# Performance work log

Measured on AMD Instinct MI355X. Metric: run time of the kernel, lower is better.

Reference implementation:

```python
import jax, jax.numpy as jnp
import numpy as np

NUM_HEADS = 12
D_MODEL = 768
D_K = D_MODEL // NUM_HEADS


def setup_inputs() -> dict:
    key = jax.random.key(0)
    k0, k1, k2, k3, k4 = jax.random.split(key, 5)
    B, S = 4, 2048
    scale = 1.0 / np.sqrt(D_MODEL)
    return {
        "x": jax.random.normal(k0, (B, S, D_MODEL), dtype=jnp.float32),
        "wq": jax.random.normal(k1, (D_MODEL, D_MODEL), dtype=jnp.float32) * scale,
        "wk": jax.random.normal(k2, (D_MODEL, D_MODEL), dtype=jnp.float32) * scale,
        "wv": jax.random.normal(k3, (D_MODEL, D_MODEL), dtype=jnp.float32) * scale,
        "wo": jax.random.normal(k4, (D_MODEL, D_MODEL), dtype=jnp.float32) * scale,
    }


def reference(x, wq, wk, wv, wo):
    # x: [B, S, d_model]; weights are torch Linear weights [out, in], applied as x @ W^T
    B, S, _ = x.shape
    q = (x @ wq.T).reshape(B, S, NUM_HEADS, D_K).transpose(0, 2, 1, 3)  # [B,H,S,dk]
    k = (x @ wk.T).reshape(B, S, NUM_HEADS, D_K).transpose(0, 2, 1, 3)
    v = (x @ wv.T).reshape(B, S, NUM_HEADS, D_K).transpose(0, 2, 1, 3)
    # Note: original calls scaled_dot_product_attention(queries, keys, values),
    # whose body computes (first_arg @ second_arg^T) => standard Q K^T scores.
    scores = jnp.einsum("bhqd,bhkd->bhqk", q, k) / jnp.sqrt(jnp.float32(D_K))
    causal_mask = jnp.triu(jnp.ones((S, S), dtype=bool), k=1)  # True above diagonal
    scores = jnp.where(causal_mask, -jnp.inf, scores)
    probs = jax.nn.softmax(scores, axis=-1)  # stable max-subtracted softmax, as in source
    attn = jnp.einsum("bhqk,bhkd->bhqd", probs, v)  # [B,H,S,dk]
    attn = attn.transpose(0, 2, 1, 3).reshape(B, S, D_MODEL)
    return attn @ wo.T
```

## Files before the change

kernel.cpp:

```cpp
#include <hip/hip_runtime.h>
#include <stdint.h>

#define DMODEL 768
#define NHEADS 12
#define DK 64
#define BATCH 4
#define SEQ 2048
#define MTOK (BATCH*SEQ)

typedef float f32x4 __attribute__((ext_vector_type(4)));
typedef short bf16x8 __attribute__((ext_vector_type(8)));
typedef unsigned short u16;

__device__ __forceinline__ u16 f2bf(float f) {
  uint32_t u = __float_as_uint(f);
  u += 0x7FFFu + ((u >> 16) & 1u);
  return (u16)(u >> 16);
}

#define GLDS16(g, l) __builtin_amdgcn_global_load_lds( \
    (const __attribute__((address_space(1))) unsigned int*)(g), \
    (__attribute__((address_space(3))) unsigned int*)(l), 16, 0, 0)

__global__ void cvt_kernel(const float* __restrict__ src, u16* __restrict__ dst, int n4) {
  int i = blockIdx.x * blockDim.x + threadIdx.x;
  if (i >= n4) return;
  float4 v = reinterpret_cast<const float4*>(src)[i];
  ushort4 o;
  o.x = f2bf(v.x); o.y = f2bf(v.y); o.z = f2bf(v.z); o.w = f2bf(v.w);
  reinterpret_cast<ushort4*>(dst)[i] = o;
}

__global__ void cvt_w4(const float* __restrict__ w0, const float* __restrict__ w1,
                       const float* __restrict__ w2, const float* __restrict__ w3,
                       u16* __restrict__ dst, int n4) {
  int i = blockIdx.x * blockDim.x + threadIdx.x;
  if (i >= n4) return;
  const float* src = (blockIdx.y == 0) ? w0 : (blockIdx.y == 1) ? w1 : (blockIdx.y == 2) ? w2 : w3;
  float4 v = reinterpret_cast<const float4*>(src)[i];
  ushort4 o;
  o.x = f2bf(v.x); o.y = f2bf(v.y); o.z = f2bf(v.z); o.w = f2bf(v.w);
  reinterpret_cast<ushort4*>(dst + (size_t)blockIdx.y * DMODEL * DMODEL)[i] = o;
}

#define BM 128
#define BN 128
#define BK 32

__device__ __forceinline__ void gemm_loop(const u16* __restrict__ A, const u16* __restrict__ W,
                                          int bm, int bn, int t, u16* As, u16* Ws,
                                          f32x4 (&acc)[2][4]) {
  const int lane = t & 63;
  const int wave = t >> 6;
  const int r16 = lane & 15, g = lane >> 4;
  const int wr = (wave >> 1) * 32;
  const int wc = (wave & 1) * 64;
  const int crow = t >> 2;
  const int cchunk = (t & 3) ^ ((t >> 3) & 3);
  const size_t aoff = (size_t)(bm + crow) * DMODEL + cchunk * 8;
  const size_t woff = (size_t)(bn + crow) * DMODEL + cchunk * 8;

  GLDS16(A + aoff, As + t * 8);
  GLDS16(W + woff, Ws + t * 8);
  __syncthreads();

  const int NK = DMODEL / BK;
  for (int kt = 0; kt < NK; ++kt) {
    const int cur = kt & 1;
    if (kt + 1 < NK) {
      GLDS16(A + aoff + (size_t)(kt + 1) * BK, As + (cur ^ 1) * 4096 + t * 8);
      GLDS16(W + woff + (size_t)(kt + 1) * BK, Ws + (cur ^ 1) * 4096 + t * 8);
    }
    bf16x8 af[2], bfr[4];
#pragma unroll
    for (int m = 0; m < 2; ++m) {
      const int row = wr + m * 16 + r16;
      af[m] = *reinterpret_cast<const bf16x8*>(&As[cur * 4096 + row * 32 + ((g ^ ((row >> 1) & 3)) * 8)]);
    }
#pragma unroll
    for (int n = 0; n < 4; ++n) {
      const int row = wc + n * 16 + r16;
      bfr[n] = *reinterpret_cast<const bf16x8*>(&Ws[cur * 4096 + row * 32 + ((g ^ ((row >> 1) & 3)) * 8)]);
    }
#pragma unroll
    for (int m = 0; m < 2; ++m)
#pragma unroll
      for (int n = 0; n < 4; ++n)
        acc[m][n] = __builtin_amdgcn_mfma_f32_16x16x32_bf16(af[m], bfr[n], acc[m][n], 0, 0, 0);
    __syncthreads();
  }
}

__launch_bounds__(512)
__global__ void qkv_gemm(const u16* __restrict__ A, const u16* __restrict__ wAll,
                         u16* __restrict__ Qw, u16* __restrict__ Kw, u16* __restrict__ Vtw) {
  __shared__ __align__(16) u16 As[2 * BM * BK];
  __shared__ __align__(16) u16 Ws[2 * BN * BK];
  const int t = threadIdx.x;
  const int lane = t & 63, wave = t >> 6;
  const int r16 = lane & 15, g = lane >> 4;
  const int bm = blockIdx.x * BM, bn = blockIdx.y * BN;
  const int z = blockIdx.z;
  const u16* W = wAll + (size_t)z * DMODEL * DMODEL;
  const int wr = (wave >> 1) * 32, wc = (wave & 1) * 64;

  f32x4 acc[2][4] = {};
  gemm_loop(A, W, bm, bn, t, As, Ws, acc);

  if (z <= 1) {
    u16* Qo = (z == 0) ? Qw : Kw;
    const float scl = (z == 0) ? 0.125f : 1.0f;
#pragma unroll
    for (int m = 0; m < 2; ++m) {
      const int gi0 = bm + wr + m * 16 + g * 4;
#pragma unroll
      for (int n = 0; n < 4; ++n) {
        const int gj = bn + wc + n * 16 + r16;
        const int h = gj >> 6, dc = gj & 63;
#pragma unroll
        for (int r = 0; r < 4; ++r) {
          const int gi = gi0 + r;
          const int b_ = gi >> 11, s = gi & 2047;
          Qo[((size_t)((b_ * NHEADS + h) * SEQ + s) << 6) + dc] = f2bf(acc[m][n][r] * scl);
        }
      }
    }
  } else {
#pragma unroll
    for (int m = 0; m < 2; ++m) {
      const int gi0 = bm + wr + m * 16 + g * 4;
      const int b_ = gi0 >> 11, s0 = gi0 & 2047;
#pragma unroll
      for (int n = 0; n < 4; ++n) {
        const int gj = bn + wc + n * 16 + r16;
        const int h = gj >> 6, dc = gj & 63;
        ushort4 pk;
        pk.x = f2bf(acc[m][n][0]); pk.y = f2bf(acc[m][n][1]);
        pk.z = f2bf(acc[m][n][2]); pk.w = f2bf(acc[m][n][3]);
        *reinterpret_cast<ushort4*>(Vtw + ((size_t)((b_ * NHEADS + h) * DK + dc) * SEQ + s0)) = pk;
      }
    }
  }
}

__launch_bounds__(512)
__global__ void out_gemm(const u16* __restrict__ A, const u16* __restrict__ W,
                         float* __restrict__ C) {
  __shared__ __align__(16) u16 As[2 * BM * BK];
  __shared__ __align__(16) u16 Ws[2 * BN * BK];
  const int t = threadIdx.x;
  const int lane = t & 63, wave = t >> 6;
  const int r16 = lane & 15, g = lane >> 4;
  const int bm = blockIdx.x * BM, bn = blockIdx.y * BN;
  const int wr = (wave >> 1) * 32, wc = (wave & 1) * 64;

  f32x4 acc[2][4] = {};
  gemm_loop(A, W, bm, bn, t, As, Ws, acc);

#pragma unroll
  for (int m = 0; m < 2; ++m) {
    const int gi0 = bm + wr + m * 16 + g * 4;
#pragma unroll
    for (int n = 0; n < 4; ++n) {
      const int gj = bn + wc + n * 16 + r16;
#pragma unroll
      for (int r = 0; r < 4; ++r)
        C[(size_t)(gi0 + r) * DMODEL + gj] = acc[m][n][r];
    }
  }
}

__launch_bounds__(256)
__global__ void attn_kernel(const u16* __restrict__ Qg, const u16* __restrict__ Kg,
                            const u16* __restrict__ Vtg, u16* __restrict__ Og) {
  __shared__ __align__(16) u16 Ks[2][64 * 64];
  __shared__ __align__(16) u16 Vt[2][64 * 64];
  __shared__ __align__(16) u16 Ps[4 * 16 * 64];
  const int t = threadIdx.x;
  const int lane = t & 63, wave = t >> 6;
  const int r16 = lane & 15, g = lane >> 4;
  const int bx = blockIdx.x;
  const int qt = 31 - (bx / 48);
  const int hb = bx % 48;
  const int h = hb % NHEADS, b = hb / NHEADS;
  const int q0 = qt * 64;
  const int ntot = qt + 1;
  const size_t bh = (size_t)(b * NHEADS + h);
  const u16* Qb = Qg + bh * SEQ * DK;
  const u16* Kb = Kg + bh * SEQ * DK;
  const u16* Vb = Vtg + bh * DK * SEQ;

  const int sr0 = t >> 3, sc = (t & 7) * 8, sr1 = sr0 + 32;
  const int kp0 = ((sr0 & 15) << 2) | (sr0 >> 4);
  const int kp1 = ((sr1 & 15) << 2) | (sr1 >> 4);

  bf16x8 aq[2];
  const int qrow = q0 + wave * 16 + r16;
#pragma unroll
  for (int kc = 0; kc < 2; ++kc)
    aq[kc] = *reinterpret_cast<const bf16x8*>(Qb + (size_t)qrow * DK + kc * 32 + g * 8);

  f32x4 o[4] = {};
  float mrun[4], lrun[4];
#pragma unroll
  for (int r = 0; r < 4; ++r) { mrun[r] = -__builtin_inff(); lrun[r] = 0.f; }

  const int qrbase = q0 + wave * 16 + g * 4;
  const int kvb = r16 * 4;

  {
    uint4 k0 = *reinterpret_cast<const uint4*>(Kb + (size_t)kp0 * DK + sc);
    uint4 k1 = *reinterpret_cast<const uint4*>(Kb + (size_t)kp1 * DK + sc);
    uint4 v0 = *reinterpret_cast<const uint4*>(Vb + (size_t)sr0 * SEQ + sc);
    uint4 v1 = *reinterpret_cast<const uint4*>(Vb + (size_t)sr1 * SEQ + sc);
    *reinterpret_cast<uint4*>((char*)Ks[0] + ((sr0 * 128 + sc * 2) ^ ((sr0 & 7) << 4))) = k0;
    *reinterpret_cast<uint4*>((char*)Ks[0] + ((sr1 * 128 + sc * 2) ^ ((sr1 & 7) << 4))) = k1;
    *reinterpret_cast<uint4*>((char*)Vt[0] + ((sr0 * 128 + sc * 2) ^ ((sr0 & 7) << 4))) = v0;
    *reinterpret_cast<uint4*>((char*)Vt[0] + ((sr1 * 128 + sc * 2) ^ ((sr1 & 7) << 4))) = v1;
  }
  __syncthreads();

  for (int i = 0; i < ntot; ++i) {
    const int cur = i & 1;
    const int kv0 = i * 64;
    const bool nx = (i + 1 < ntot);
    uint4 kn0, kn1, vn0, vn1;
    if (nx) {
      const int nkv0 = kv0 + 64;
      kn0 = *reinterpret_cast<const uint4*>(Kb + (size_t)(nkv0 + kp0) * DK + sc);
      kn1 = *reinterpret_cast<const uint4*>(Kb + (size_t)(nkv0 + kp1) * DK + sc);
      vn0 = *reinterpret_cast<const uint4*>(Vb + (size_t)sr0 * SEQ + nkv0 + sc);
      vn1 = *reinterpret_cast<const uint4*>(Vb + (size_t)sr1 * SEQ + nkv0 + sc);
    }

    f32x4 sfr[4];
#pragma unroll
    for (int nb = 0; nb < 4; ++nb) {
      f32x4 a = {};
#pragma unroll
      for (int kc = 0; kc < 2; ++kc) {
        const int row = nb * 16 + r16;
        bf16x8 bk = *reinterpret_cast<const bf16x8*>(
            (char*)Ks[cur] + ((row * 128 + kc * 64 + g * 16) ^ ((row & 7) << 4)));
        a = __builtin_amdgcn_mfma_f32_16x16x32_bf16(aq[kc], bk, a, 0, 0, 0);
      }
      sfr[nb] = a;
    }

    const bool diag = (i == qt);
#pragma unroll
    for (int r = 0; r < 4; ++r) {
      const int qr = qrbase + r;
      float sv[4];
#pragma unroll
      for (int nb = 0; nb < 4; ++nb) {
        float xs = sfr[nb][r];
        if (diag && (kv0 + kvb + nb > qr)) xs = -__builtin_inff();
        sv[nb] = xs;
      }
      float mt = fmaxf(fmaxf(sv[0], sv[1]), fmaxf(sv[2], sv[3]));
#pragma unroll
      for (int mm = 1; mm < 16; mm <<= 1) mt = fmaxf(mt, __shfl_xor(mt, mm));
      if (!__all(mt <= mrun[r])) {
        const float mnew = fmaxf(mrun[r], mt);
        const float corr = __expf(mrun[r] - mnew);
        lrun[r] *= corr;
#pragma unroll
        for (int ob = 0; ob < 4; ++ob) o[ob][r] *= corr;
        mrun[r] = mnew;
      }
      const float m_ = mrun[r];
      const float p0 = __expf(sv[0] - m_), p1 = __expf(sv[1] - m_);
      const float p2 = __expf(sv[2] - m_), p3 = __expf(sv[3] - m_);
      float psum = (p0 + p1) + (p2 + p3);
#pragma unroll
      for (int mm = 1; mm < 16; mm <<= 1) psum += __shfl_xor(psum, mm);
      lrun[r] += psum;
      uint32_t lo, hi;
      asm("v_cvt_pk_bf16_f32 %0, %1, %2" : "=v"(lo) : "v"(p0), "v"(p1));
      asm("v_cvt_pk_bf16_f32 %0, %1, %2" : "=v"(hi) : "v"(p2), "v"(p3));
      const int prow = g * 4 + r;
      *reinterpret_cast<uint2*>((char*)Ps + wave * 2048 +
          ((prow * 128 + r16 * 8) ^ ((prow & 7) << 4))) = uint2{lo, hi};
    }

#pragma unroll
    for (int kc = 0; kc < 2; ++kc) {
      bf16x8 pa = *reinterpret_cast<const bf16x8*>((char*)Ps + wave * 2048 +
          ((r16 * 128 + kc * 64 + g * 16) ^ ((r16 & 7) << 4)));
#pragma unroll
      for (int ob = 0; ob < 4; ++ob) {
        const int vrow = ob * 16 + r16;
        bf16x8 bv = *reinterpret_cast<const bf16x8*>(
            (char*)Vt[cur] + ((vrow * 128 + kc * 64 + g * 16) ^ ((vrow & 7) << 4)));
        o[ob] = __builtin_amdgcn_mfma_f32_16x16x32_bf16(pa, bv, o[ob], 0, 0, 0);
      }
    }

    if (nx) {
      const int nb_ = cur ^ 1;
      *reinterpret_cast<uint4*>((char*)Ks[nb_] + ((sr0 * 128 + sc * 2) ^ ((sr0 & 7) << 4))) = kn0;
      *reinterpret_cast<uint4*>((char*)Ks[nb_] + ((sr1 * 128 + sc * 2) ^ ((sr1 & 7) << 4))) = kn1;
      *reinterpret_cast<uint4*>((char*)Vt[nb_] + ((sr0 * 128 + sc * 2) ^ ((sr0 & 7) << 4))) = vn0;
      *reinterpret_cast<uint4*>((char*)Vt[nb_] + ((sr1 * 128 + sc * 2) ^ ((sr1 & 7) << 4))) = vn1;
    }
    __syncthreads();
  }

  const int tok0 = b * SEQ + q0 + wave * 16 + g * 4;
#pragma unroll
  for (int r = 0; r < 4; ++r) {
    const float rinv = 1.0f / lrun[r];
#pragma unroll
    for (int ob = 0; ob < 4; ++ob)
      Og[(size_t)(tok0 + r) * DMODEL + h * 64 + ob * 16 + r16] = f2bf(o[ob][r] * rinv);
  }
}

extern "C" void kernel_launch(void* const* d_in, const int* in_sizes, int n_in,
                              void* d_out, int out_size, void* d_ws, size_t ws_size,
                              hipStream_t stream) {
  const float* x  = (const float*)d_in[0];
  const float* wq = (const float*)d_in[1];
  const float* wk = (const float*)d_in[2];
  const float* wv = (const float*)d_in[3];
  const float* wo = (const float*)d_in[4];

  const size_t SZ_TOK = (size_t)MTOK * DMODEL * 2;
  const size_t SZ_W   = (size_t)DMODEL * DMODEL * 2;
  char* ws = (char*)d_ws;
  size_t off = 0;
  u16* xb  = (u16*)(ws + off); off += SZ_TOK;
  u16* wqb = (u16*)(ws + off); off += 4 * SZ_W;
  u16* Qw  = (u16*)(ws + off); off += SZ_TOK;
  u16* Kw  = (u16*)(ws + off); off += SZ_TOK;
  u16* Vtw = (u16*)(ws + off); off += SZ_TOK;
  u16* Ow  = (u16*)(ws + off); off += SZ_TOK;
  if (ws_size < off) return;
  u16* wob = wqb + 3 * (size_t)DMODEL * DMODEL;

  const int nx4 = MTOK * DMODEL / 4;
  const int nw4 = DMODEL * DMODEL / 4;
  cvt_kernel<<<nx4 / 256, 256, 0, stream>>>(x, xb, nx4);
  cvt_w4<<<dim3(nw4 / 256, 4), 256, 0, stream>>>(wq, wk, wv, wo, wqb, nw4);

  qkv_gemm<<<dim3(MTOK / BM, DMODEL / BN, 3), 512, 0, stream>>>(xb, wqb, Qw, Kw, Vtw);

  attn_kernel<<<dim3(1536), 256, 0, stream>>>(Qw, Kw, Vtw, Ow);

  out_gemm<<<dim3(MTOK / BM, DMODEL / BN), 512, 0, stream>>>(Ow, wob, (float*)d_out);
}
```

Baseline: 243.0 us.

## Rewrite attention with 32x32 MFMA, register-resident P, and async LDS loads

The attention kernel now computes transposed score tiles S^T = K·Q^T with 32x32x16 MFMAs, so each lane owns one query row. The P fragment for the PV MFMA is built in registers by packing to bf16 and swapping halves across lanes with shuffles, which removes the per-tile shared-memory round trip for P. Each block now covers 128 queries (4 waves of 32) and loads K/V tiles with global_load_lds double buffering instead of staging them through registers. Per-row max and sum reductions shrink to a single cross-half shuffle. In exchange the grid halves to 768 blocks and each wave holds more registers, which may reduce occupancy and parallelism.

```diff
diff --git a/kernel.cpp b/kernel.cpp
--- a/kernel.cpp
+++ b/kernel.cpp
@@ -9,8 +9,10 @@
 #define MTOK (BATCH*SEQ)
 
 typedef float f32x4 __attribute__((ext_vector_type(4)));
+typedef float f32x16 __attribute__((ext_vector_type(16)));
 typedef short bf16x8 __attribute__((ext_vector_type(8)));
 typedef unsigned short u16;
+typedef unsigned int u32;
 
 __device__ __forceinline__ u16 f2bf(float f) {
   uint32_t u = __float_as_uint(f);
@@ -170,150 +172,173 @@
   }
 }
 
-__launch_bounds__(256)
+__device__ __forceinline__ bf16x8 mk_pa(int hi, float p0, float p1, float p2, float p3,
+                                        float p4, float p5, float p6, float p7) {
+  u32 w01, w23, w45, w67;
+  asm("v_cvt_pk_bf16_f32 %0, %1, %2" : "=v"(w01) : "v"(p0), "v"(p1));
+  asm("v_cvt_pk_bf16_f32 %0, %1, %2" : "=v"(w23) : "v"(p2), "v"(p3));
+  asm("v_cvt_pk_bf16_f32 %0, %1, %2" : "=v"(w45) : "v"(p4), "v"(p5));
+  asm("v_cvt_pk_bf16_f32 %0, %1, %2" : "=v"(w67) : "v"(p6), "v"(p7));
+  const u32 pw01 = (u32)__shfl_xor((int)w01, 32);
+  const u32 pw23 = (u32)__shfl_xor((int)w23, 32);
+  const u32 pw45 = (u32)__shfl_xor((int)w45, 32);
+  const u32 pw67 = (u32)__shfl_xor((int)w67, 32);
+  union { u32 w[4]; bf16x8 v; } u;
+  u.w[0] = hi ? pw45 : w01;
+  u.w[1] = hi ? pw67 : w23;
+  u.w[2] = hi ? w45  : pw01;
+  u.w[3] = hi ? w67  : pw23;
+  return u.v;
+}
+
+__launch_bounds__(256, 2)
 __global__ void attn_kernel(const u16* __restrict__ Qg, const u16* __restrict__ Kg,
                             const u16* __restrict__ Vtg, u16* __restrict__ Og) {
   __shared__ __align__(16) u16 Ks[2][64 * 64];
-  __shared__ __align__(16) u16 Vt[2][64 * 64];
-  __shared__ __align__(16) u16 Ps[4 * 16 * 64];
+  __shared__ __align__(16) u16 Vs[2][64 * 64];
   const int t = threadIdx.x;
-  const int lane = t & 63, wave = t >> 6;
-  const int r16 = lane & 15, g = lane >> 4;
+  const int lane = t & 63, warp = t >> 6;
+  const int l31 = lane & 31, hi = lane >> 5;
   const int bx = blockIdx.x;
-  const int qt = 31 - (bx / 48);
+  const int qt = 15 - (bx / 48);
   const int hb = bx % 48;
   const int h = hb % NHEADS, b = hb / NHEADS;
-  const int q0 = qt * 64;
-  const int ntot = qt + 1;
+  const int q0w = qt * 128 + warp * 32;
+  const int nt = 2 * qt + 2;
   const size_t bh = (size_t)(b * NHEADS + h);
   const u16* Qb = Qg + bh * SEQ * DK;
   const u16* Kb = Kg + bh * SEQ * DK;
   const u16* Vb = Vtg + bh * DK * SEQ;
 
-  const int sr0 = t >> 3, sc = (t & 7) * 8, sr1 = sr0 + 32;
-  const int kp0 = ((sr0 & 15) << 2) | (sr0 >> 4);
-  const int kp1 = ((sr1 & 15) << 2) | (sr1 >> 4);
-
-  bf16x8 aq[2];
-  const int qrow = q0 + wave * 16 + r16;
-#pragma unroll
-  for (int kc = 0; kc < 2; ++kc)
-    aq[kc] = *reinterpret_cast<const bf16x8*>(Qb + (size_t)qrow * DK + kc * 32 + g * 8);
-
-  f32x4 o[4] = {};
-  float mrun[4], lrun[4];
-#pragma unroll
-  for (int r = 0; r < 4; ++r) { mrun[r] = -__builtin_inff(); lrun[r] = 0.f; }
-
-  const int qrbase = q0 + wave * 16 + g * 4;
-  const int kvb = r16 * 4;
-
-  {
-    uint4 k0 = *reinterpret_cast<const uint4*>(Kb + (size_t)kp0 * DK + sc);
-    uint4 k1 = *reinterpret_cast<const uint4*>(Kb + (size_t)kp1 * DK + sc);
-    uint4 v0 = *reinterpret_cast<const uint4*>(Vb + (size_t)sr0 * SEQ + sc);
-    uint4 v1 = *reinterpret_cast<const uint4*>(Vb + (size_t)sr1 * SEQ + sc);
-    *reinterpret_cast<uint4*>((char*)Ks[0] + ((sr0 * 128 + sc * 2) ^ ((sr0 & 7) << 4))) = k0;
-    *reinterpret_cast<uint4*>((char*)Ks[0] + ((sr1 * 128 + sc * 2) ^ ((sr1 & 7) << 4))) = k1;
-    *reinterpret_cast<uint4*>((char*)Vt[0] + ((sr0 * 128 + sc * 2) ^ ((sr0 & 7) << 4))) = v0;
-    *reinterpret_cast<uint4*>((char*)Vt[0] + ((sr1 * 128 + sc * 2) ^ ((sr1 & 7) << 4))) = v1;
+  int srow[2], scol[2];
+#pragma unroll
+  for (int j = 0; j < 2; ++j) {
+    const int bb = (t + j * 256) * 16;
+    srow[j] = bb >> 7;
+    scol[j] = ((bb & 127) ^ ((srow[j] & 7) << 4)) >> 1;
+  }
+
+  const int q = q0w + l31;
+  bf16x8 qf[4];
+#pragma unroll
+  for (int kk = 0; kk < 4; ++kk)
+    qf[kk] = *reinterpret_cast<const bf16x8*>(Qb + (size_t)q * DK + kk * 16 + hi * 8);
+
+  f32x16 o0 = {}, o1 = {};
+  float m = -__builtin_inff(), l = 0.f;
+  const int hi4 = hi * 4;
+  const int xr = (l31 & 7) << 4;
+
+#pragma unroll
+  for (int j = 0; j < 2; ++j) {
+    GLDS16(Kb + (size_t)srow[j] * DK + scol[j], &Ks[0][0] + (t + j * 256) * 8);
+    GLDS16(Vb + (size_t)srow[j] * SEQ + scol[j], &Vs[0][0] + (t + j * 256) * 8);
   }
   __syncthreads();
 
-  for (int i = 0; i < ntot; ++i) {
+  for (int i = 0; i < nt; ++i) {
     const int cur = i & 1;
     const int kv0 = i * 64;
-    const bool nx = (i + 1 < ntot);
-    uint4 kn0, kn1, vn0, vn1;
-    if (nx) {
+    if (i + 1 < nt) {
       const int nkv0 = kv0 + 64;
-      kn0 = *reinterpret_cast<const uint4*>(Kb + (size_t)(nkv0 + kp0) * DK + sc);
-      kn1 = *reinterpret_cast<const uint4*>(Kb + (size_t)(nkv0 + kp1) * DK + sc);
-      vn0 = *reinterpret_cast<const uint4*>(Vb + (size_t)sr0 * SEQ + nkv0 + sc);
-      vn1 = *reinterpret_cast<const uint4*>(Vb + (size_t)sr1 * SEQ + nkv0 + sc);
-    }
-
-    f32x4 sfr[4];
-#pragma unroll
-    for (int nb = 0; nb < 4; ++nb) {
-      f32x4 a = {};
-#pragma unroll
-      for (int kc = 0; kc < 2; ++kc) {
-        const int row = nb * 16 + r16;
-        bf16x8 bk = *reinterpret_cast<const bf16x8*>(
-            (char*)Ks[cur] + ((row * 128 + kc * 64 + g * 16) ^ ((row & 7) << 4)));
-        a = __builtin_amdgcn_mfma_f32_16x16x32_bf16(aq[kc], bk, a, 0, 0, 0);
-      }
-      sfr[nb] = a;
-    }
-
-    const bool diag = (i == qt);
-#pragma unroll
-    for (int r = 0; r < 4; ++r) {
-      const int qr = qrbase + r;
-      float sv[4];
-#pragma unroll
-      for (int nb = 0; nb < 4; ++nb) {
-        float xs = sfr[nb][r];
-        if (diag && (kv0 + kvb + nb > qr)) xs = -__builtin_inff();
-        sv[nb] = xs;
-      }
-      float mt = fmaxf(fmaxf(sv[0], sv[1]), fmaxf(sv[2], sv[3]));
-#pragma unroll
-      for (int mm = 1; mm < 16; mm <<= 1) mt = fmaxf(mt, __shfl_xor(mt, mm));
-      if (!__all(mt <= mrun[r])) {
-        const float mnew = fmaxf(mrun[r], mt);
-        const float corr = __expf(mrun[r] - mnew);
-        lrun[r] *= corr;
-#pragma unroll
-        for (int ob = 0; ob < 4; ++ob) o[ob][r] *= corr;
-        mrun[r] = mnew;
-      }
-      const float m_ = mrun[r];
-      const float p0 = __expf(sv[0] - m_), p1 = __expf(sv[1] - m_);
-      const float p2 = __expf(sv[2] - m_), p3 = __expf(sv[3] - m_);
-      float psum = (p0 + p1) + (p2 + p3);
-#pragma unroll
-      for (int mm = 1; mm < 16; mm <<= 1) psum += __shfl_xor(psum, mm);
-      lrun[r] += psum;
-      uint32_t lo, hi;
-      asm("v_cvt_pk_bf16_f32 %0, %1, %2" : "=v"(lo) : "v"(p0), "v"(p1));
-      asm("v_cvt_pk_bf16_f32 %0, %1, %2" : "=v"(hi) : "v"(p2), "v"(p3));
-      const int prow = g * 4 + r;
-      *reinterpret_cast<uint2*>((char*)Ps + wave * 2048 +
-          ((prow * 128 + r16 * 8) ^ ((prow & 7) << 4))) = uint2{lo, hi};
-    }
-
-#pragma unroll
-    for (int kc = 0; kc < 2; ++kc) {
-      bf16x8 pa = *reinterpret_cast<const bf16x8*>((char*)Ps + wave * 2048 +
-          ((r16 * 128 + kc * 64 + g * 16) ^ ((r16 & 7) << 4)));
-#pragma unroll
-      for (int ob = 0; ob < 4; ++ob) {
-        const int vrow = ob * 16 + r16;
-        bf16x8 bv = *reinterpret_cast<const bf16x8*>(
-            (char*)Vt[cur] + ((vrow * 128 + kc * 64 + g * 16) ^ ((vrow & 7) << 4)));
-        o[ob] = __builtin_amdgcn_mfma_f32_16x16x32_bf16(pa, bv, o[ob], 0, 0, 0);
-      }
-    }
-
-    if (nx) {
-      const int nb_ = cur ^ 1;
-      *reinterpret_cast<uint4*>((char*)Ks[nb_] + ((sr0 * 128 + sc * 2) ^ ((sr0 & 7) << 4))) = kn0;
-      *reinterpret_cast<uint4*>((char*)Ks[nb_] + ((sr1 * 128 + sc * 2) ^ ((sr1 & 7) << 4))) = kn1;
-      *reinterpret_cast<uint4*>((char*)Vt[nb_] + ((sr0 * 128 + sc * 2) ^ ((sr0 & 7) << 4))) = vn0;
-      *reinterpret_cast<uint4*>((char*)Vt[nb_] + ((sr1 * 128 + sc * 2) ^ ((sr1 & 7) << 4))) = vn1;
+#pragma unroll
+      for (int j = 0; j < 2; ++j) {
+        GLDS16(Kb + (size_t)(nkv0 + srow[j]) * DK + scol[j], &Ks[cur ^ 1][0] + (t + j * 256) * 8);
+        GLDS16(Vb + (size_t)srow[j] * SEQ + nkv0 + scol[j], &Vs[cur ^ 1][0] + (t + j * 256) * 8);
+      }
+    }
+
+    if (kv0 <= q0w + 31) {
+      f32x16 t0 = {}, t1 = {};
+      const char* Kc = (const char*)Ks[cur];
+#pragma unroll
+      for (int kk = 0; kk < 4; ++kk) {
+        const int cb = kk * 32 + hi * 16;
+        bf16x8 a0 = *reinterpret_cast<const bf16x8*>(Kc + ((l31 * 128 + cb) ^ xr));
+        bf16x8 a1 = *reinterpret_cast<const bf16x8*>(Kc + (((l31 + 32) * 128 + cb) ^ xr));
+        t0 = __builtin_amdgcn_mfma_f32_32x32x16_bf16(a0, qf[kk], t0, 0, 0, 0);
+        t1 = __builtin_amdgcn_mfma_f32_32x32x16_bf16(a1, qf[kk], t1, 0, 0, 0);
+      }
+
+      if (kv0 + 63 > q0w) {
+        const int qmh = (q - kv0) - hi4;
+#pragma unroll
+        for (int r = 0; r < 16; ++r) {
+          const int kvc = (r & 3) + 8 * (r >> 2);
+          if (kvc > qmh)      t0[r] = -__builtin_inff();
+          if (kvc + 32 > qmh) t1[r] = -__builtin_inff();
+        }
+      }
+
+      float x0 = fmaxf(t0[0], t0[1]),  x1 = fmaxf(t0[2], t0[3]);
+      float x2 = fmaxf(t0[4], t0[5]),  x3 = fmaxf(t0[6], t0[7]);
+      float x4 = fmaxf(t0[8], t0[9]),  x5 = fmaxf(t0[10], t0[11]);
+      float x6 = fmaxf(t0[12], t0[13]), x7 = fmaxf(t0[14], t0[15]);
+      x0 = fmaxf(x0, x1); x2 = fmaxf(x2, x3); x4 = fmaxf(x4, x5); x6 = fmaxf(x6, x7);
+      float y0 = fmaxf(t1[0], t1[1]),  y1 = fmaxf(t1[2], t1[3]);
+      float y2 = fmaxf(t1[4], t1[5]),  y3 = fmaxf(t1[6], t1[7]);
+      float y4 = fmaxf(t1[8], t1[9]),  y5 = fmaxf(t1[10], t1[11]);
+      float y6 = fmaxf(t1[12], t1[13]), y7 = fmaxf(t1[14], t1[15]);
+      y0 = fmaxf(y0, y1); y2 = fmaxf(y2, y3); y4 = fmaxf(y4, y5); y6 = fmaxf(y6, y7);
+      float pm = fmaxf(fmaxf(fmaxf(x0, x2), fmaxf(x4, x6)),
+                       fmaxf(fmaxf(y0, y2), fmaxf(y4, y6)));
+      pm = fmaxf(pm, __shfl_xor(pm, 32));
+
+      if (pm > m) {
+        const float corr = __expf(m - pm);
+        l *= corr;
+        o0 = o0 * corr;
+        o1 = o1 * corr;
+        m = pm;
+      }
+
+#pragma unroll
+      for (int r = 0; r < 16; ++r) { t0[r] = __expf(t0[r] - m); }
+#pragma unroll
+      for (int r = 0; r < 16; ++r) { t1[r] = __expf(t1[r] - m); }
+      float s0 = 0.f, s1 = 0.f, s2 = 0.f, s3 = 0.f;
+#pragma unroll
+      for (int r = 0; r < 4; ++r) {
+        s0 += t0[r]; s1 += t0[4 + r]; s2 += t0[8 + r]; s3 += t0[12 + r];
+        s0 += t1[r]; s1 += t1[4 + r]; s2 += t1[8 + r]; s3 += t1[12 + r];
+      }
+      float s = (s0 + s1) + (s2 + s3);
+      l += s + __shfl_xor(s, 32);
+
+      bf16x8 pa0 = mk_pa(hi, t0[0], t0[1], t0[2], t0[3], t0[4], t0[5], t0[6], t0[7]);
+      bf16x8 pa1 = mk_pa(hi, t0[8], t0[9], t0[10], t0[11], t0[12], t0[13], t0[14], t0[15]);
+      bf16x8 pa2 = mk_pa(hi, t1[0], t1[1], t1[2], t1[3], t1[4], t1[5], t1[6], t1[7]);
+      bf16x8 pa3 = mk_pa(hi, t1[8], t1[9], t1[10], t1[11], t1[12], t1[13], t1[14], t1[15]);
+
+      const char* Vc = (const char*)Vs[cur];
+#pragma unroll
+      for (int ks = 0; ks < 4; ++ks) {
+        const int cb = ks * 32 + hi * 16;
+        bf16x8 v0 = *reinterpret_cast<const bf16x8*>(Vc + ((l31 * 128 + cb) ^ xr));
+        bf16x8 v1 = *reinterpret_cast<const bf16x8*>(Vc + (((l31 + 32) * 128 + cb) ^ xr));
+        const bf16x8 pk = (ks == 0) ? pa0 : (ks == 1) ? pa1 : (ks == 2) ? pa2 : pa3;
+        o0 = __builtin_amdgcn_mfma_f32_32x32x16_bf16(v0, pk, o0, 0, 0, 0);
+        o1 = __builtin_amdgcn_mfma_f32_32x32x16_bf16(v1, pk, o1, 0, 0, 0);
+      }
     }
     __syncthreads();
   }
 
-  const int tok0 = b * SEQ + q0 + wave * 16 + g * 4;
-#pragma unroll
-  for (int r = 0; r < 4; ++r) {
-    const float rinv = 1.0f / lrun[r];
-#pragma unroll
-    for (int ob = 0; ob < 4; ++ob)
-      Og[(size_t)(tok0 + r) * DMODEL + h * 64 + ob * 16 + r16] = f2bf(o[ob][r] * rinv);
+  const float rinv = 1.0f / l;
+  u16* orow = Og + (size_t)(b * SEQ + q) * DMODEL + h * 64;
+#pragma unroll
+  for (int j = 0; j < 4; ++j) {
+    ushort4 pk;
+    pk.x = f2bf(o0[4 * j + 0] * rinv); pk.y = f2bf(o0[4 * j + 1] * rinv);
+    pk.z = f2bf(o0[4 * j + 2] * rinv); pk.w = f2bf(o0[4 * j + 3] * rinv);
+    *reinterpret_cast<ushort4*>(orow + 8 * j + hi4) = pk;
+  }
+#pragma unroll
+  for (int j = 0; j < 4; ++j) {
+    ushort4 pk;
+    pk.x = f2bf(o1[4 * j + 0] * rinv); pk.y = f2bf(o1[4 * j + 1] * rinv);
+    pk.z = f2bf(o1[4 * j + 2] * rinv); pk.w = f2bf(o1[4 * j + 3] * rinv);
+    *reinterpret_cast<ushort4*>(orow + 32 + 8 * j + hi4) = pk;
   }
 }
 
@@ -346,7 +371,7 @@
 
   qkv_gemm<<<dim3(MTOK / BM, DMODEL / BN, 3), 512, 0, stream>>>(xb, wqb, Qw, Kw, Vtw);
 
-  attn_kernel<<<dim3(1536), 256, 0, stream>>>(Qw, Kw, Vtw, Ow);
+  attn_kernel<<<dim3(768), 256, 0, stream>>>(Qw, Kw, Vtw, Ow);
 
   out_gemm<<<dim3(MTOK / BM, DMODEL / BN), 512, 0, stream>>>(Ow, wob, (float*)d_out);
 }
```

Result: faster. 205.6 us (-15.4%).
